# Optimization experiments

Hardware: AMD Instinct MI355X
Metric: run time of the kernel (lower is better)

The kernel has to match this reference:

```python
import jax, jax.numpy as jnp
import numpy as np
from jax import lax

# --- static config (mirrors DecodeDetectionsFast __init__) ---
CONF_THRESH = 0.01
IOU_THRESH = 0.45
TOP_K = 200
NMS_MAX = 400
IMG_H = 512.0
IMG_W = 512.0
NEG = -1e10  # sentinel for suppressed / invalid scores


def setup_inputs() -> dict:
    key = jax.random.key(0)
    # (batch, n_boxes, n_classes + 12); last 12 = [offsets(4), anchors(4), variances(4)]
    y_pred = jax.random.normal(key, (32, 24564, 93), dtype=jnp.float32)
    return {"y_pred": y_pred}


def _iou_one_vs_all(box, boxes):
    # box: (4,) [xmin,ymin,xmax,ymax]; boxes: (N,4). TF-style IoU (no area clamp,
    # intersection clamped at 0).
    ix1 = jnp.maximum(box[0], boxes[:, 0])
    iy1 = jnp.maximum(box[1], boxes[:, 1])
    ix2 = jnp.minimum(box[2], boxes[:, 2])
    iy2 = jnp.minimum(box[3], boxes[:, 3])
    inter = jnp.maximum(ix2 - ix1, 0.0) * jnp.maximum(iy2 - iy1, 0.0)
    area = (box[2] - box[0]) * (box[3] - box[1])
    areas = (boxes[:, 2] - boxes[:, 0]) * (boxes[:, 3] - boxes[:, 1])
    union = area + areas - inter
    return jnp.where(union > 0.0, inter / union, 0.0)


def _nms_topk_one(preds, scores):
    # preds: (N,6) rows [class_id, conf, xmin, ymin, xmax, ymax]; scores: (N,)
    boxes = preds[:, 2:6]

    def step(sc, _):
        i = jnp.argmax(sc)
        s = sc[i]
        sel_valid = s > NEG * 0.5
        iou = _iou_one_vs_all(boxes[i], boxes)
        sc_new = jnp.where(iou > IOU_THRESH, NEG, sc).at[i].set(NEG)
        sc_new = jnp.where(sel_valid, sc_new, sc)
        return sc_new, (i, sel_valid)

    _, (idxs, valid) = lax.scan(step, scores, None, length=NMS_MAX)
    cand = preds[idxs] * valid[:, None].astype(preds.dtype)  # (NMS_MAX, 6); invalid -> zero rows
    _, top_idx = lax.top_k(cand[:, 1], TOP_K)  # sort by confidence, zero-padded rows sink
    return cand[top_idx]


def reference(y_pred):
    n_classes = y_pred.shape[2] - 12
    cls_scores = y_pred[..., :n_classes]
    class_ids = jnp.argmax(cls_scores, axis=-1).astype(y_pred.dtype)  # (B,N)
    conf = jnp.max(cls_scores, axis=-1)  # (B,N)

    # decode centroid offsets with anchors and variances
    cx = y_pred[..., -12] * y_pred[..., -4] * y_pred[..., -6] + y_pred[..., -8]
    cy = y_pred[..., -11] * y_pred[..., -3] * y_pred[..., -5] + y_pred[..., -7]
    w = jnp.exp(y_pred[..., -10] * y_pred[..., -2]) * y_pred[..., -6]
    h = jnp.exp(y_pred[..., -9] * y_pred[..., -1]) * y_pred[..., -5]

    xmin = (cx - 0.5 * w) * IMG_W
    ymin = (cy - 0.5 * h) * IMG_H
    xmax = (cx + 0.5 * w) * IMG_W
    ymax = (cy + 0.5 * h) * IMG_H

    preds = jnp.stack([class_ids, conf, xmin, ymin, xmax, ymax], axis=-1)  # (B,N,6)

    # background (class 0) removal + confidence thresholding via score masking
    valid = (class_ids != 0.0) & (conf > CONF_THRESH)
    scores = jnp.where(valid, conf, NEG)

    return jax.vmap(_nms_topk_one)(preds, scores)  # (B, TOP_K, 6)
```

## Files before the change

### kernel.cpp

```cpp
#include <hip/hip_runtime.h>
#include <stdint.h>

#define NANCH 24564
#define NBATCH 32
#define NCLS 81
#define FEAT 93
#define NEGV -10000000000.0f
#define CONF_T 0.01f
#define IOU_T 0.45f
#define TOPK 200
#define CAP 1024
#define TARGET 768u
#define NBINS 1024
#define APB 64
#define NF4 (APB * FEAT / 4)

__global__ __launch_bounds__(256) void decode_kernel(
    const float* __restrict__ yp, float4* __restrict__ boxes,
    float* __restrict__ scores, float* __restrict__ cls) {
#pragma clang fp contract(off)
  __shared__ float lds[APB * FEAT];
  const float* src = yp + (size_t)blockIdx.x * (APB * FEAT);

  for (int i = threadIdx.x; i < NF4; i += 256) {
    int wb = i & ~63;
    __builtin_amdgcn_global_load_lds(
        (const __attribute__((address_space(1))) void*)(src + (size_t)i * 4),
        (__attribute__((address_space(3))) void*)(lds + wb * 4),
        16, 0, 0);
  }
  __syncthreads();

  const int L = threadIdx.x;
  const int a = L >> 2;
  const int part = L & 3;
  const float* p = &lds[a * FEAT];

  int c0 = part * 21;
  int c1 = (part == 3) ? NCLS : c0 + 21;
  float best = -3.0e38f;
  int bi = c0;
  for (int c = c0; c < c1; ++c) {
    float v = p[c];
    if (v > best) { best = v; bi = c; }
  }
  for (int off = 1; off < 4; off <<= 1) {
    float ov = __shfl_xor(best, off, 64);
    int   oi = __shfl_xor(bi, off, 64);
    if (ov > best || (ov == best && oi < bi)) { best = ov; bi = oi; }
  }

  if (part == 0) {
    float cx = p[81] * p[89] * p[87] + p[85];
    float cy = p[82] * p[90] * p[88] + p[86];
    float w  = expf(p[83] * p[91]) * p[87];
    float h  = expf(p[84] * p[92]) * p[88];
    float xmin = (cx - 0.5f * w) * 512.0f;
    float ymin = (cy - 0.5f * h) * 512.0f;
    float xmax = (cx + 0.5f * w) * 512.0f;
    float ymax = (cy + 0.5f * h) * 512.0f;
    int ga = blockIdx.x * APB + a;
    boxes[ga] = make_float4(xmin, ymin, xmax, ymax);
    cls[ga] = (float)bi;
    scores[ga] = (bi != 0 && best > CONF_T) ? best : NEGV;
  }
}

__device__ __forceinline__ bool iou_gt(float sx1, float sy1, float sx2, float sy2,
                                       float bx1, float by1, float bx2, float by2) {
#pragma clang fp contract(off)
  float ix1 = fmaxf(sx1, bx1);
  float iy1 = fmaxf(sy1, by1);
  float ix2 = fminf(sx2, bx2);
  float iy2 = fminf(sy2, by2);
  float inter = fmaxf(ix2 - ix1, 0.0f) * fmaxf(iy2 - iy1, 0.0f);
  float area_s = (sx2 - sx1) * (sy2 - sy1);
  float area_b = (bx2 - bx1) * (by2 - by1);
  float uni = area_s + area_b - inter;
  float iou = (uni > 0.0f) ? (inter / uni) : 0.0f;
  return iou > IOU_T;
}

__device__ __forceinline__ unsigned long long maxu64(unsigned long long a, unsigned long long b) { return a > b ? a : b; }
__device__ __forceinline__ unsigned long long minu64(unsigned long long a, unsigned long long b) { return a < b ? a : b; }

__global__ __launch_bounds__(1024) void nms_kernel(
    const float4* __restrict__ boxes, const float* __restrict__ scores,
    const float* __restrict__ cls, float* __restrict__ out) {
#pragma clang fp contract(off)
  __shared__ unsigned long long keys[CAP];
  __shared__ float4 cbox[CAP];
  __shared__ unsigned int hist[NBINS];
  __shared__ float selb[TOPK * 5];
  __shared__ unsigned int sel_idx[TOPK];
  __shared__ float sel_score[TOPK];
  __shared__ unsigned int s_cnt;
  __shared__ int s_cutoff;
  __shared__ int s_nsel;

  const int b = blockIdx.x;
  const int tid = threadIdx.x;
  const size_t base = (size_t)b * NANCH;

  float sreg[24];
#pragma unroll
  for (int j = 0; j < 24; ++j) {
    int i = tid + j * 1024;
    sreg[j] = (i < NANCH) ? scores[base + i] : NEGV;
  }

  hist[tid] = 0u;
  if (tid == 0) { s_cnt = 0u; s_cutoff = 0; s_nsel = 0; }
  __syncthreads();
#pragma unroll
  for (int j = 0; j < 24; ++j) {
    float s = sreg[j];
    if (s >= 0.0f) {
      int bin = (int)(s * ((float)NBINS / 6.0f));
      bin = bin > (NBINS - 1) ? (NBINS - 1) : bin;
      atomicAdd(&hist[bin], 1u);
    }
  }
  __syncthreads();

  if (tid < 64) {
    int lane = tid;
    unsigned int h[16];
    unsigned int S = 0;
#pragma unroll
    for (int t = 0; t < 16; ++t) { h[t] = hist[lane * 16 + t]; S += h[t]; }
    unsigned int incl = S;
    for (int off = 1; off < 64; off <<= 1) {
      unsigned int o = __shfl_down(incl, off, 64);
      if (lane + off < 64) incl += o;
    }
    unsigned int acc = incl - S;
#pragma unroll
    for (int t = 15; t >= 0; --t) { acc += h[t]; hist[lane * 16 + t] = acc; }
  }
  __syncthreads();
  {
    unsigned int sfx = hist[tid];
    unsigned int nxt = (tid < NBINS - 1) ? hist[tid + 1] : 0u;
    if (sfx >= TARGET && nxt < TARGET) s_cutoff = tid;
  }
  __syncthreads();
  float cutoffv = (float)s_cutoff * (6.0f / (float)NBINS);

#pragma unroll
  for (int j = 0; j < 24; ++j) {
    float s = sreg[j];
    if (s >= cutoffv) {
      unsigned int pos = atomicAdd(&s_cnt, 1u);
      if (pos < CAP) {
        unsigned int i = (unsigned int)(tid + j * 1024);
        keys[pos] = ((unsigned long long)__float_as_uint(s) << 32) |
                    (unsigned long long)(~i);
      }
    }
  }
  __syncthreads();
  int cnt = (int)(s_cnt > CAP ? CAP : s_cnt);

  unsigned long long v = (tid < cnt) ? keys[tid] : 0ull;
  for (int k = 2; k <= 64; k <<= 1) {
    for (int j = k >> 1; j >= 1; j >>= 1) {
      unsigned long long o = __shfl_xor((long long)v, j, 64);
      bool keepmax = (((tid & k) == 0) == ((tid & j) == 0));
      v = keepmax ? maxu64(v, o) : minu64(v, o);
    }
  }
  for (int k = 128; k <= CAP; k <<= 1) {
    for (int j = k >> 1; j >= 64; j >>= 1) {
      keys[tid] = v;
      __syncthreads();
      unsigned long long o = keys[tid ^ j];
      bool keepmax = (((tid & k) == 0) == ((tid & j) == 0));
      v = keepmax ? maxu64(v, o) : minu64(v, o);
      __syncthreads();
    }
    for (int j = 32; j >= 1; j >>= 1) {
      unsigned long long o = __shfl_xor((long long)v, j, 64);
      bool keepmax = (((tid & k) == 0) == ((tid & j) == 0));
      v = keepmax ? maxu64(v, o) : minu64(v, o);
    }
  }
  keys[tid] = v;
  __syncthreads();

  if (v != 0ull) {
    unsigned int idx = ~(unsigned int)(v & 0xFFFFFFFFull);
    cbox[tid] = boxes[base + idx];
  }
  __syncthreads();

  if (tid < 64) {
    int lane = tid;
    float b0x=0,b0y=0,b0z=0,b0w=0, b1x=0,b1y=0,b1z=0,b1w=0;
    float b2x=0,b2y=0,b2z=0,b2w=0, b3x=0,b3y=0,b3z=0,b3w=0;
    unsigned int i0=0,i1=0,i2=0,i3=0;
    float s0=0,s1=0,s2=0,s3=0;
    int nsel = 0;
    unsigned long long nkey = keys[0];
    float4 nbox = cbox[0];
    for (int c = 0; c < cnt && nsel < TOPK; ++c) {
      unsigned long long key = nkey;
      float4 box = nbox;
      int cn = (c + 1 < cnt) ? c + 1 : c;
      nkey = keys[cn];
      nbox = cbox[cn];
      bool sup = false;
      if (lane < nsel)       sup |= iou_gt(b0x,b0y,b0z,b0w, box.x,box.y,box.z,box.w);
      if (64 + lane < nsel)  sup |= iou_gt(b1x,b1y,b1z,b1w, box.x,box.y,box.z,box.w);
      if (128 + lane < nsel) sup |= iou_gt(b2x,b2y,b2z,b2w, box.x,box.y,box.z,box.w);
      if (192 + lane < nsel) sup |= iou_gt(b3x,b3y,b3z,b3w, box.x,box.y,box.z,box.w);
      if (!__any(sup ? 1 : 0)) {
        if (lane == (nsel & 63)) {
          unsigned int idx = ~(unsigned int)(key & 0xFFFFFFFFull);
          float sc = __uint_as_float((unsigned int)(key >> 32));
          int slot = nsel >> 6;
          if (slot == 0)      { b0x=box.x; b0y=box.y; b0z=box.z; b0w=box.w; i0=idx; s0=sc; }
          else if (slot == 1) { b1x=box.x; b1y=box.y; b1z=box.z; b1w=box.w; i1=idx; s1=sc; }
          else if (slot == 2) { b2x=box.x; b2y=box.y; b2z=box.z; b2w=box.w; i2=idx; s2=sc; }
          else                { b3x=box.x; b3y=box.y; b3z=box.z; b3w=box.w; i3=idx; s3=sc; }
        }
        nsel++;
      }
    }
    if (lane < nsel)       { int r = lane;     selb[r*5+0]=b0x; selb[r*5+1]=b0y; selb[r*5+2]=b0z; selb[r*5+3]=b0w; sel_idx[r]=i0; sel_score[r]=s0; }
    if (64 + lane < nsel)  { int r = 64+lane;  selb[r*5+0]=b1x; selb[r*5+1]=b1y; selb[r*5+2]=b1z; selb[r*5+3]=b1w; sel_idx[r]=i1; sel_score[r]=s1; }
    if (128 + lane < nsel) { int r = 128+lane; selb[r*5+0]=b2x; selb[r*5+1]=b2y; selb[r*5+2]=b2z; selb[r*5+3]=b2w; sel_idx[r]=i2; sel_score[r]=s2; }
    if (192 + lane < nsel) { int r = 192+lane; selb[r*5+0]=b3x; selb[r*5+1]=b3y; selb[r*5+2]=b3z; selb[r*5+3]=b3w; sel_idx[r]=i3; sel_score[r]=s3; }
    if (lane == 0) s_nsel = nsel;
  }
  __syncthreads();

  int nsel = s_nsel;
  for (int e = tid; e < TOPK * 6; e += 1024) {
    int r = e / 6, col = e % 6;
    float val = 0.0f;
    if (r < nsel) {
      if (col == 0)      val = cls[base + sel_idx[r]];
      else if (col == 1) val = sel_score[r];
      else               val = selb[r * 5 + (col - 2)];
    }
    out[(size_t)b * (TOPK * 6) + e] = val;
  }
}

extern "C" void kernel_launch(void* const* d_in, const int* in_sizes, int n_in,
                              void* d_out, int out_size, void* d_ws, size_t ws_size,
                              hipStream_t stream) {
  const float* yp = (const float*)d_in[0];
  float* out = (float*)d_out;
  char* ws = (char*)d_ws;

  const int total_anch = NANCH * NBATCH;
  float4* boxes = (float4*)ws;
  float* scores = (float*)(ws + (size_t)total_anch * 16);
  float* cls    = (float*)(ws + (size_t)total_anch * 16 + (size_t)total_anch * 4);

  const int nblk = total_anch / APB;
  decode_kernel<<<nblk, 256, 0, stream>>>(yp, boxes, scores, cls);
  nms_kernel<<<NBATCH, 1024, 0, stream>>>(boxes, scores, cls, out);
}
```

Baseline: 491.4 us.

## Process two NMS candidates per iteration and replace IoU division with multiply-compare

```diff
diff --git a/kernel.cpp b/kernel.cpp
--- a/kernel.cpp
+++ b/kernel.cpp
@@ -66,19 +66,17 @@
   }
 }
 
-__device__ __forceinline__ bool iou_gt(float sx1, float sy1, float sx2, float sy2,
-                                       float bx1, float by1, float bx2, float by2) {
+__device__ __forceinline__ bool iou_chk(float sx1, float sy1, float sx2, float sy2, float sarea,
+                                        float bx1, float by1, float bx2, float by2, float barea) {
 #pragma clang fp contract(off)
   float ix1 = fmaxf(sx1, bx1);
   float iy1 = fmaxf(sy1, by1);
   float ix2 = fminf(sx2, bx2);
   float iy2 = fminf(sy2, by2);
   float inter = fmaxf(ix2 - ix1, 0.0f) * fmaxf(iy2 - iy1, 0.0f);
-  float area_s = (sx2 - sx1) * (sy2 - sy1);
-  float area_b = (bx2 - bx1) * (by2 - by1);
-  float uni = area_s + area_b - inter;
-  float iou = (uni > 0.0f) ? (inter / uni) : 0.0f;
-  return iou > IOU_T;
+  float uni = sarea + barea - inter;
+  const double UMID = 0.5 * ((double)0.45f + (double)__uint_as_float(0x3EE66667u));
+  return (uni > 0.0f) && ((double)inter > UMID * (double)uni);
 }
 
 __device__ __forceinline__ unsigned long long maxu64(unsigned long long a, unsigned long long b) { return a > b ? a : b; }
@@ -198,35 +196,70 @@
     int lane = tid;
     float b0x=0,b0y=0,b0z=0,b0w=0, b1x=0,b1y=0,b1z=0,b1w=0;
     float b2x=0,b2y=0,b2z=0,b2w=0, b3x=0,b3y=0,b3z=0,b3w=0;
+    float ar0=0, ar1=0, ar2=0, ar3=0;
     unsigned int i0=0,i1=0,i2=0,i3=0;
     float s0=0,s1=0,s2=0,s3=0;
     int nsel = 0;
-    unsigned long long nkey = keys[0];
-    float4 nbox = cbox[0];
-    for (int c = 0; c < cnt && nsel < TOPK; ++c) {
-      unsigned long long key = nkey;
-      float4 box = nbox;
-      int cn = (c + 1 < cnt) ? c + 1 : c;
-      nkey = keys[cn];
-      nbox = cbox[cn];
-      bool sup = false;
-      if (lane < nsel)       sup |= iou_gt(b0x,b0y,b0z,b0w, box.x,box.y,box.z,box.w);
-      if (64 + lane < nsel)  sup |= iou_gt(b1x,b1y,b1z,b1w, box.x,box.y,box.z,box.w);
-      if (128 + lane < nsel) sup |= iou_gt(b2x,b2y,b2z,b2w, box.x,box.y,box.z,box.w);
-      if (192 + lane < nsel) sup |= iou_gt(b3x,b3y,b3z,b3w, box.x,box.y,box.z,box.w);
-      if (!__any(sup ? 1 : 0)) {
-        if (lane == (nsel & 63)) {
-          unsigned int idx = ~(unsigned int)(key & 0xFFFFFFFFull);
-          float sc = __uint_as_float((unsigned int)(key >> 32));
-          int slot = nsel >> 6;
-          if (slot == 0)      { b0x=box.x; b0y=box.y; b0z=box.z; b0w=box.w; i0=idx; s0=sc; }
-          else if (slot == 1) { b1x=box.x; b1y=box.y; b1z=box.z; b1w=box.w; i1=idx; s1=sc; }
-          else if (slot == 2) { b2x=box.x; b2y=box.y; b2z=box.z; b2w=box.w; i2=idx; s2=sc; }
-          else                { b3x=box.x; b3y=box.y; b3z=box.z; b3w=box.w; i3=idx; s3=sc; }
-        }
-        nsel++;
+
+    auto insert_sel = [&](unsigned long long key, float4 box, float area) {
+      if (lane == (nsel & 63)) {
+        unsigned int idx = ~(unsigned int)(key & 0xFFFFFFFFull);
+        float sc = __uint_as_float((unsigned int)(key >> 32));
+        int slot = nsel >> 6;
+        if (slot == 0)      { b0x=box.x; b0y=box.y; b0z=box.z; b0w=box.w; ar0=area; i0=idx; s0=sc; }
+        else if (slot == 1) { b1x=box.x; b1y=box.y; b1z=box.z; b1w=box.w; ar1=area; i1=idx; s1=sc; }
+        else if (slot == 2) { b2x=box.x; b2y=box.y; b2z=box.z; b2w=box.w; ar2=area; i2=idx; s2=sc; }
+        else                { b3x=box.x; b3y=box.y; b3z=box.z; b3w=box.w; ar3=area; i3=idx; s3=sc; }
       }
-    }
+      nsel++;
+    };
+
+    if (cnt > 0) {
+      unsigned long long kA = keys[0], kB;
+      float4 bA = cbox[0], bB;
+      { int j1 = (1 < cnt) ? 1 : 0; kB = keys[j1]; bB = cbox[j1]; }
+      for (int c = 0; c < cnt && nsel < TOPK; c += 2) {
+        unsigned long long keyA = kA; float4 boxA = bA;
+        unsigned long long keyB = kB; float4 boxB = bB;
+        int p2 = (c + 2 < cnt) ? c + 2 : 0;
+        int p3 = (c + 3 < cnt) ? c + 3 : 0;
+        kA = keys[p2]; bA = cbox[p2];
+        kB = keys[p3]; bB = cbox[p3];
+        bool hasB = (c + 1 < cnt);
+        float areaA = (boxA.z - boxA.x) * (boxA.w - boxA.y);
+        float areaB = (boxB.z - boxB.x) * (boxB.w - boxB.y);
+        bool supA = false, supB = false;
+        if (lane < nsel) {
+          supA |= iou_chk(b0x,b0y,b0z,b0w,ar0, boxA.x,boxA.y,boxA.z,boxA.w,areaA);
+          supB |= iou_chk(b0x,b0y,b0z,b0w,ar0, boxB.x,boxB.y,boxB.z,boxB.w,areaB);
+        }
+        if (64 + lane < nsel) {
+          supA |= iou_chk(b1x,b1y,b1z,b1w,ar1, boxA.x,boxA.y,boxA.z,boxA.w,areaA);
+          supB |= iou_chk(b1x,b1y,b1z,b1w,ar1, boxB.x,boxB.y,boxB.z,boxB.w,areaB);
+        }
+        if (128 + lane < nsel) {
+          supA |= iou_chk(b2x,b2y,b2z,b2w,ar2, boxA.x,boxA.y,boxA.z,boxA.w,areaA);
+          supB |= iou_chk(b2x,b2y,b2z,b2w,ar2, boxB.x,boxB.y,boxB.z,boxB.w,areaB);
+        }
+        if (192 + lane < nsel) {
+          supA |= iou_chk(b3x,b3y,b3z,b3w,ar3, boxA.x,boxA.y,boxA.z,boxA.w,areaA);
+          supB |= iou_chk(b3x,b3y,b3z,b3w,ar3, boxB.x,boxB.y,boxB.z,boxB.w,areaB);
+        }
+        bool selA   = !__any(supA ? 1 : 0);
+        bool supBany = __any(supB ? 1 : 0);
+        if (selA) {
+          insert_sel(keyA, boxA, areaA);
+          if (hasB && nsel < TOPK) {
+            bool ab = iou_chk(boxA.x,boxA.y,boxA.z,boxA.w, areaA,
+                              boxB.x,boxB.y,boxB.z,boxB.w, areaB);
+            if (!supBany && !ab) insert_sel(keyB, boxB, areaB);
+          }
+        } else {
+          if (hasB && !supBany) insert_sel(keyB, boxB, areaB);
+        }
+      }
+    }
+
     if (lane < nsel)       { int r = lane;     selb[r*5+0]=b0x; selb[r*5+1]=b0y; selb[r*5+2]=b0z; selb[r*5+3]=b0w; sel_idx[r]=i0; sel_score[r]=s0; }
     if (64 + lane < nsel)  { int r = 64+lane;  selb[r*5+0]=b1x; selb[r*5+1]=b1y; selb[r*5+2]=b1z; selb[r*5+3]=b1w; sel_idx[r]=i1; sel_score[r]=s1; }
     if (128 + lane < nsel) { int r = 128+lane; selb[r*5+0]=b2x; selb[r*5+1]=b2y; selb[r*5+2]=b2z; selb[r*5+3]=b2w; sel_idx[r]=i2; sel_score[r]=s2; }
```

Result: slower. 514.5 us (+4.7%).

## Replace serial per-candidate NMS loop with tiled IoU bitmask resolution

Applied to the files above, without the earlier changes.

```diff
diff --git a/kernel.cpp b/kernel.cpp
--- a/kernel.cpp
+++ b/kernel.cpp
@@ -91,6 +91,8 @@
   __shared__ unsigned long long keys[CAP];
   __shared__ float4 cbox[CAP];
   __shared__ unsigned int hist[NBINS];
+  __shared__ unsigned long long tmat[256 * 4];
+  __shared__ unsigned char psup4[4][256];
   __shared__ float selb[TOPK * 5];
   __shared__ unsigned int sel_idx[TOPK];
   __shared__ float sel_score[TOPK];
@@ -194,46 +196,90 @@
   }
   __syncthreads();
 
-  if (tid < 64) {
-    int lane = tid;
-    float b0x=0,b0y=0,b0z=0,b0w=0, b1x=0,b1y=0,b1z=0,b1w=0;
-    float b2x=0,b2y=0,b2z=0,b2w=0, b3x=0,b3y=0,b3z=0,b3w=0;
-    unsigned int i0=0,i1=0,i2=0,i3=0;
-    float s0=0,s1=0,s2=0,s3=0;
-    int nsel = 0;
-    unsigned long long nkey = keys[0];
-    float4 nbox = cbox[0];
-    for (int c = 0; c < cnt && nsel < TOPK; ++c) {
-      unsigned long long key = nkey;
-      float4 box = nbox;
-      int cn = (c + 1 < cnt) ? c + 1 : c;
-      nkey = keys[cn];
-      nbox = cbox[cn];
+  for (int t = 0; t < 4; ++t) {
+    int lo = t * 256;
+    if (lo >= cnt) break;
+    int tlen = cnt - lo; if (tlen > 256) tlen = 256;
+    int nprior = s_nsel;
+    if (nprior >= TOPK) break;
+
+    {
+      int c = tid & 255;
+      int s0 = tid >> 8;
       bool sup = false;
-      if (lane < nsel)       sup |= iou_gt(b0x,b0y,b0z,b0w, box.x,box.y,box.z,box.w);
-      if (64 + lane < nsel)  sup |= iou_gt(b1x,b1y,b1z,b1w, box.x,box.y,box.z,box.w);
-      if (128 + lane < nsel) sup |= iou_gt(b2x,b2y,b2z,b2w, box.x,box.y,box.z,box.w);
-      if (192 + lane < nsel) sup |= iou_gt(b3x,b3y,b3z,b3w, box.x,box.y,box.z,box.w);
-      if (!__any(sup ? 1 : 0)) {
-        if (lane == (nsel & 63)) {
-          unsigned int idx = ~(unsigned int)(key & 0xFFFFFFFFull);
-          float sc = __uint_as_float((unsigned int)(key >> 32));
-          int slot = nsel >> 6;
-          if (slot == 0)      { b0x=box.x; b0y=box.y; b0z=box.z; b0w=box.w; i0=idx; s0=sc; }
-          else if (slot == 1) { b1x=box.x; b1y=box.y; b1z=box.z; b1w=box.w; i1=idx; s1=sc; }
-          else if (slot == 2) { b2x=box.x; b2y=box.y; b2z=box.z; b2w=box.w; i2=idx; s2=sc; }
-          else                { b3x=box.x; b3y=box.y; b3z=box.z; b3w=box.w; i3=idx; s3=sc; }
+      if (c < tlen && nprior > 0) {
+        float4 cb = cbox[lo + c];
+        for (int s = s0; s < nprior; s += 4)
+          sup |= iou_gt(selb[s * 5 + 0], selb[s * 5 + 1],
+                        selb[s * 5 + 2], selb[s * 5 + 3],
+                        cb.x, cb.y, cb.z, cb.w);
+      }
+      psup4[s0][c] = sup ? (unsigned char)1 : (unsigned char)0;
+    }
+
+    {
+      int w = tid >> 8;
+      int j = tid & 255;
+      unsigned long long bits = 0ull;
+      if (j < tlen) {
+        float4 bj = cbox[lo + j];
+        int ibeg = w * 64;
+        int iend = ibeg + 64; if (iend > j) iend = j;
+        for (int i = ibeg; i < iend; ++i) {
+          float4 bi = cbox[lo + i];
+          if (iou_gt(bi.x, bi.y, bi.z, bi.w, bj.x, bj.y, bj.z, bj.w))
+            bits |= 1ull << (i & 63);
         }
-        nsel++;
       }
-    }
-    if (lane < nsel)       { int r = lane;     selb[r*5+0]=b0x; selb[r*5+1]=b0y; selb[r*5+2]=b0z; selb[r*5+3]=b0w; sel_idx[r]=i0; sel_score[r]=s0; }
-    if (64 + lane < nsel)  { int r = 64+lane;  selb[r*5+0]=b1x; selb[r*5+1]=b1y; selb[r*5+2]=b1z; selb[r*5+3]=b1w; sel_idx[r]=i1; sel_score[r]=s1; }
-    if (128 + lane < nsel) { int r = 128+lane; selb[r*5+0]=b2x; selb[r*5+1]=b2y; selb[r*5+2]=b2z; selb[r*5+3]=b2w; sel_idx[r]=i2; sel_score[r]=s2; }
-    if (192 + lane < nsel) { int r = 192+lane; selb[r*5+0]=b3x; selb[r*5+1]=b3y; selb[r*5+2]=b3z; selb[r*5+3]=b3w; sel_idx[r]=i3; sel_score[r]=s3; }
-    if (lane == 0) s_nsel = nsel;
-  }
-  __syncthreads();
+      tmat[j * 4 + w] = bits;
+    }
+    __syncthreads();
+
+    if (tid < 64) {
+      int lane = tid;
+      unsigned long long m0 = 0ull, m1 = 0ull, m2 = 0ull, m3 = 0ull;
+      int nsel = nprior;
+
+#define RESOLVE_SLOT(SLOT, MWORD)                                              \
+      if ((SLOT) * 64 < tlen && nsel < TOPK) {                                 \
+        const int cbase = (SLOT) * 64;                                         \
+        unsigned long long ra = tmat[(cbase + lane) * 4 + 0];                  \
+        unsigned long long rb = tmat[(cbase + lane) * 4 + 1];                  \
+        unsigned long long rc = tmat[(cbase + lane) * 4 + 2];                  \
+        unsigned long long rd = tmat[(cbase + lane) * 4 + 3];                  \
+        bool mypsup = (psup4[0][cbase + lane] | psup4[1][cbase + lane] |       \
+                       psup4[2][cbase + lane] | psup4[3][cbase + lane]) != 0;  \
+        int cend = tlen - cbase; if (cend > 64) cend = 64;                     \
+        for (int cc = 0; cc < cend && nsel < TOPK; ++cc) {                     \
+          bool sup = mypsup |                                                  \
+              (((ra & m0) | (rb & m1) | (rc & m2) | (rd & m3)) != 0ull);       \
+          unsigned long long voted = __ballot(sup ? 1 : 0);                    \
+          if (!((voted >> cc) & 1ull)) {                                       \
+            MWORD |= 1ull << cc;                                               \
+            if (lane == cc) {                                                  \
+              int gc = lo + cbase + cc;                                        \
+              float4 bx = cbox[gc];                                            \
+              unsigned long long key = keys[gc];                               \
+              selb[nsel * 5 + 0] = bx.x; selb[nsel * 5 + 1] = bx.y;            \
+              selb[nsel * 5 + 2] = bx.z; selb[nsel * 5 + 3] = bx.w;            \
+              sel_idx[nsel]   = ~(unsigned int)(key & 0xFFFFFFFFull);          \
+              sel_score[nsel] = __uint_as_float((unsigned int)(key >> 32));    \
+            }                                                                  \
+            nsel++;                                                            \
+          }                                                                    \
+        }                                                                      \
+      }
+
+      RESOLVE_SLOT(0, m0)
+      RESOLVE_SLOT(1, m1)
+      RESOLVE_SLOT(2, m2)
+      RESOLVE_SLOT(3, m3)
+#undef RESOLVE_SLOT
+
+      if (lane == 0) s_nsel = nsel;
+    }
+    __syncthreads();
+  }
 
   int nsel = s_nsel;
   for (int e = tid; e < TOPK * 6; e += 1024) {
```

Measured after the change: 446.5 us. 9.1% less time.
